# Optimization experiments

Hardware: AMD Instinct MI355X
Metric: run time of the kernel (lower is better)

The kernel has to match this reference:

```python
import jax, jax.numpy as jnp
import numpy as np

B, S, I, H = 64, 2048, 256, 256


def setup_inputs() -> dict:
    key = jax.random.key(0)
    ks = jax.random.split(key, 13)
    s_i = 1.0 / np.sqrt(I)
    s_h = 1.0 / np.sqrt(H)
    inp = {
        "input_seq": jax.random.normal(ks[0], (B, S, I), dtype=jnp.float32),
        "Wz": jax.random.uniform(ks[1], (I, H), jnp.float32, -s_i, s_i),
        "bz": jax.random.uniform(ks[2], (H,), jnp.float32, -s_i, s_i),
        "Wr": jax.random.uniform(ks[3], (I, H), jnp.float32, -s_i, s_i),
        "br": jax.random.uniform(ks[4], (H,), jnp.float32, -s_i, s_i),
        "Wh": jax.random.uniform(ks[5], (I, H), jnp.float32, -s_i, s_i),
        "bh": jax.random.uniform(ks[6], (H,), jnp.float32, -s_i, s_i),
        "Uz": jax.random.uniform(ks[7], (H, H), jnp.float32, -s_h, s_h),
        "buz": jax.random.uniform(ks[8], (H,), jnp.float32, -s_h, s_h),
        "Ur": jax.random.uniform(ks[9], (H, H), jnp.float32, -s_h, s_h),
        "bur": jax.random.uniform(ks[10], (H,), jnp.float32, -s_h, s_h),
        "Uh": jax.random.uniform(ks[11], (H, H), jnp.float32, -s_h, s_h),
        "buh": jax.random.uniform(ks[12], (H,), jnp.float32, -s_h, s_h),
    }
    return inp


def reference(input_seq, Wz, bz, Wr, br, Wh, bh, Uz, buz, Ur, bur, Uh, buh):
    # Precompute all input-side GEMMs in one batched pass: [B,S,H] each
    xz = jnp.einsum("bsi,ih->bsh", input_seq, Wz) + bz
    xr = jnp.einsum("bsi,ih->bsh", input_seq, Wr) + br
    xh = jnp.einsum("bsi,ih->bsh", input_seq, Wh) + bh
    # Time-major for scan: [S,B,H]
    xs = (xz.transpose(1, 0, 2), xr.transpose(1, 0, 2), xh.transpose(1, 0, 2))

    def step(h_prev, x_t):
        xz_t, xr_t, xh_t = x_t
        z = jax.nn.sigmoid(xz_t + h_prev @ Uz + buz)
        r = jax.nn.sigmoid(xr_t + h_prev @ Ur + bur)
        cand = jnp.tanh(xh_t + r * (h_prev @ Uh + buh))
        h_t = (1.0 - z) * h_prev + z * cand
        return h_t, h_t

    h0 = jnp.zeros((input_seq.shape[0], Uz.shape[0]), dtype=input_seq.dtype)
    _, hs = jax.lax.scan(step, h0, xs)  # hs: [S,B,H]
    return hs.transpose(1, 0, 2)  # [B,S,H]
```

## Files before the change

kernel.cpp:

```cpp
#include <hip/hip_runtime.h>
#include <hip/hip_bf16.h>
#include <hip/hip_fp16.h>


#define S_LEN 2048
#define BATCH 64
#define HDIM  256
#define NGATE 768
#define M_TOTAL (BATCH * S_LEN)

typedef _Float16 h8_t __attribute__((ext_vector_type(8)));
typedef float    f32x4 __attribute__((ext_vector_type(4)));
typedef int      i32x4 __attribute__((ext_vector_type(4)));

static __device__ __forceinline__ float h2f(unsigned short s) {
    _Float16 h; __builtin_memcpy(&h, &s, 2); return (float)h;
}
static __device__ __forceinline__ unsigned short f2h(float f) {
    _Float16 h = (_Float16)f; unsigned short s; __builtin_memcpy(&s, &h, 2); return s;
}

static __device__ __forceinline__ float sigmoid_fast(float x) {
    float e = __builtin_amdgcn_exp2f(-1.44269504088896341f * x);
    return __builtin_amdgcn_rcpf(1.0f + e);
}
static __device__ __forceinline__ float tanh_fast(float x) {
    return 2.0f * sigmoid_fast(2.0f * x) - 1.0f;
}


__global__ void k_cvt_x(const float4* __restrict__ x4, ushort4* __restrict__ xh4) {
    int i = blockIdx.x * blockDim.x + threadIdx.x;
    float4 v = x4[i];
    ushort4 o;
    o.x = f2h(v.x); o.y = f2h(v.y); o.z = f2h(v.z); o.w = f2h(v.w);
    xh4[i] = o;
}

__global__ void k_prep_w(const float* __restrict__ Wz, const float* __restrict__ Wr,
                         const float* __restrict__ Wh,
                         const float* __restrict__ bz, const float* __restrict__ br,
                         const float* __restrict__ bh,
                         const float* __restrict__ buz, const float* __restrict__ bur,
                         unsigned short* __restrict__ Wt, float* __restrict__ biascat) {
    int n = blockIdx.x;
    int k = threadIdx.x;
    int g = n >> 8, h = n & 255;
    const float* W = (g == 0) ? Wz : (g == 1) ? Wr : Wh;
    Wt[n * 256 + k] = f2h(W[k * 256 + h]);
    if (k == 0) {
        float bias = (g == 0) ? (bz[h] + buz[h]) : (g == 1) ? (br[h] + bur[h]) : bh[h];
        biascat[n] = bias;
    }
}

__global__ void k_prep_uq(const float* __restrict__ Uz, const float* __restrict__ Ur,
                          const float* __restrict__ Uh,
                          signed char* __restrict__ Ufrag, float* __restrict__ invU) {
    int blk = blockIdx.x;
    int g = blk >> 8, col = blk & 255;
    int k = threadIdx.x;
    const float* U = (g == 0) ? Uz : (g == 1) ? Ur : Uh;
    float v = U[k * 256 + col];
    __shared__ float red[256];
    red[k] = fabsf(v);
    __syncthreads();
    for (int off = 128; off > 0; off >>= 1) {
        if (k < off) red[k] = fmaxf(red[k], red[k + off]);
        __syncthreads();
    }
    float m = red[0];
    float s = (m > 0.0f) ? 127.0f / m : 0.0f;
    int q = __float2int_rn(v * s);
    q = max(-127, min(127, q));
    int ks = k >> 6, l4 = (k >> 4) & 3, e = k & 15;
    int l = l4 * 16 + (col & 15), nt = col >> 4;
    Ufrag[((size_t)(((g * 16 + nt) * 4 + ks) * 64 + l)) * 16 + e] = (signed char)q;
    if (k == 0) invU[g * 256 + col] = m * (1.0f / 16129.0f);
}


#define LDT 264

__global__ __launch_bounds__(256) void k_gemm_x(const unsigned short* __restrict__ Xh,
                                                const unsigned short* __restrict__ Wt,
                                                const float* __restrict__ biascat,
                                                unsigned short* __restrict__ XG) {
    __shared__ unsigned short As[128 * LDT];
    __shared__ unsigned short Bs[128 * LDT];
    int tid = threadIdx.x;
    int m0 = blockIdx.x * 128;
    int n0 = blockIdx.y * 128;

    {
        const unsigned short* ga = Xh + (size_t)m0 * 256;
        const unsigned short* gb = Wt + (size_t)n0 * 256;
#pragma unroll
        for (int i = 0; i < 16; i++) {
            int chunk = tid + i * 256;
            int row = chunk >> 5;
            int c8  = (chunk & 31) * 8;
            uint4 va = *(const uint4*)(ga + row * 256 + c8);
            *(uint4*)(As + row * LDT + c8) = va;
            uint4 vb = *(const uint4*)(gb + row * 256 + c8);
            *(uint4*)(Bs + row * LDT + c8) = vb;
        }
    }
    __syncthreads();

    int lane = tid & 63, wv = tid >> 6;
    int mw = (wv & 1) * 64, nw = (wv >> 1) * 64;
    int lr = lane & 15, lg = lane >> 4;

    f32x4 acc[4][4] = {};
#pragma unroll
    for (int k = 0; k < 8; k++) {
        h8_t a[4], b[4];
#pragma unroll
        for (int i = 0; i < 4; i++)
            a[i] = *(const h8_t*)(As + (mw + i * 16 + lr) * LDT + k * 32 + lg * 8);
#pragma unroll
        for (int jj = 0; jj < 4; jj++)
            b[jj] = *(const h8_t*)(Bs + (nw + jj * 16 + lr) * LDT + k * 32 + lg * 8);
#pragma unroll
        for (int i = 0; i < 4; i++)
#pragma unroll
            for (int jj = 0; jj < 4; jj++)
                acc[i][jj] = __builtin_amdgcn_mfma_f32_16x16x32_f16(a[i], b[jj], acc[i][jj], 0, 0, 0);
    }

#pragma unroll
    for (int jj = 0; jj < 4; jj++) {
        int gcol = n0 + nw + jj * 16 + lr;
        float bias = biascat[gcol];
#pragma unroll
        for (int i = 0; i < 4; i++) {
            int grow = m0 + mw + i * 16 + lg * 4;
#pragma unroll
            for (int r = 0; r < 4; r++) {
                XG[(size_t)(grow + r) * NGATE + gcol] = f2h(acc[i][jj][r] + bias);
            }
        }
    }
}


__global__ __launch_bounds__(1024) __attribute__((amdgpu_waves_per_eu(4, 4)))
void k_gru(const i32x4* __restrict__ Ufrag,
           const float* __restrict__ invU,
           const unsigned short* __restrict__ XG,
           const float* __restrict__ buh,
           float* __restrict__ out) {
    __shared__ __align__(16) signed char hb[2][256];
    int tid = threadIdx.x;
    int lane = tid & 63, w = tid >> 6;
    int l4 = lane >> 4, lc = lane & 15;
    int b = blockIdx.x;
    int c = w * 16 + lc;

    i32x4 uf[3][4];
#pragma unroll
    for (int g = 0; g < 3; g++)
#pragma unroll
        for (int ks = 0; ks < 4; ks++)
            uf[g][ks] = Ufrag[(size_t)((g * 16 + w) * 4 + ks) * 64 + lane];
#pragma unroll
    for (int g = 0; g < 3; g++)
#pragma unroll
        for (int ks = 0; ks < 4; ks++)
            asm volatile("" : "+v"(uf[g][ks]));

    float invz = invU[0 * 256 + c], invr = invU[1 * 256 + c], invh = invU[2 * 256 + c];
    float buh_c = buh[c];

    if (tid < 128) ((int*)hb)[tid] = 0;

    const unsigned short* xb = XG + (size_t)b * S_LEN * NGATE;
    float* ob = out + (size_t)b * S_LEN * HDIM;

    unsigned short pz = xb[0 * 256 + c], pr = xb[1 * 256 + c], ph = xb[2 * 256 + c];
    float hm = 0.0f;
    __syncthreads();

    for (int t = 0; t < S_LEN; ++t) {
        int cur = t & 1;
        const signed char* hrow = hb[cur];

        i32x4 az = {}, ar = {}, ah = {};
        __builtin_amdgcn_s_setprio(1);
#pragma unroll
        for (int ks = 0; ks < 4; ks++) {
            i32x4 a = *(const i32x4*)(hrow + ks * 64 + l4 * 16);
            az = __builtin_amdgcn_mfma_i32_16x16x64_i8(a, uf[0][ks], az, 0, 0, 0);
            ar = __builtin_amdgcn_mfma_i32_16x16x64_i8(a, uf[1][ks], ar, 0, 0, 0);
            ah = __builtin_amdgcn_mfma_i32_16x16x64_i8(a, uf[2][ks], ah, 0, 0, 0);
        }
        __builtin_amdgcn_s_setprio(0);

        float z = sigmoid_fast(h2f(pz) + (float)az[0] * invz);
        float r = sigmoid_fast(h2f(pr) + (float)ar[0] * invr);
        float cd = tanh_fast(h2f(ph) + r * ((float)ah[0] * invh + buh_c));
        hm = (1.0f - z) * hm + z * cd;

        const unsigned short* xn = xb + (size_t)((t + 1 < S_LEN) ? t + 1 : t) * NGATE;
        pz = xn[0 * 256 + c]; pr = xn[1 * 256 + c]; ph = xn[2 * 256 + c];

        if (lane < 16) {
            ob[(size_t)t * HDIM + c] = hm;
            hb[cur ^ 1][c] = (signed char)__float2int_rn(hm * 127.0f);
        }
        __syncthreads();
    }
}


extern "C" void kernel_launch(void* const* d_in, const int* in_sizes, int n_in,
                              void* d_out, int out_size, void* d_ws, size_t ws_size,
                              hipStream_t stream) {
    const float* x   = (const float*)d_in[0];
    const float* Wz  = (const float*)d_in[1];
    const float* bz  = (const float*)d_in[2];
    const float* Wr  = (const float*)d_in[3];
    const float* br  = (const float*)d_in[4];
    const float* Wh  = (const float*)d_in[5];
    const float* bh  = (const float*)d_in[6];
    const float* Uz  = (const float*)d_in[7];
    const float* buz = (const float*)d_in[8];
    const float* Ur  = (const float*)d_in[9];
    const float* bur = (const float*)d_in[10];
    const float* Uh  = (const float*)d_in[11];
    const float* buh = (const float*)d_in[12];

    char* ws = (char*)d_ws;
    unsigned short* Xh = (unsigned short*)(ws);
    unsigned short* XG = (unsigned short*)(ws + 67108864);
    unsigned short* Wt = (unsigned short*)(ws + 268435456);
    signed char*    Ufrag = (signed char*)(ws + 268828672);
    float*          biascat = (float*)(ws + 269221888);
    float*          invU = (float*)(ws + 269225984);

    k_cvt_x<<<32768, 256, 0, stream>>>((const float4*)x, (ushort4*)Xh);
    k_prep_w<<<768, 256, 0, stream>>>(Wz, Wr, Wh, bz, br, bh, buz, bur, Wt, biascat);
    k_prep_uq<<<768, 256, 0, stream>>>(Uz, Ur, Uh, Ufrag, invU);

    dim3 g1(M_TOTAL / 128, NGATE / 128);
    k_gemm_x<<<g1, 256, 0, stream>>>(Xh, Wt, biascat, XG);

    k_gru<<<BATCH, 1024, 0, stream>>>((const i32x4*)Ufrag, invU, XG, buh, (float*)d_out);
}
```

Before: 1.382 ms.

## Skew GRU timestep across two wave groups to overlap gate tail with MFMA

Result: slower. 1.540 ms (+11.4%).

```diff
diff --git a/kernel.cpp b/kernel.cpp
--- a/kernel.cpp
+++ b/kernel.cpp
@@ -157,6 +157,7 @@
     int l4 = lane >> 4, lc = lane & 15;
     int b = blockIdx.x;
     int c = w * 16 + lc;
+    bool grpA = (w < 8);
 
     i32x4 uf[3][4];
 #pragma unroll
@@ -173,44 +174,77 @@
     float invz = invU[0 * 256 + c], invr = invU[1 * 256 + c], invh = invU[2 * 256 + c];
     float buh_c = buh[c];
 
-    if (tid < 128) ((int*)hb)[tid] = 0;
+    if (tid < 64) ((int*)hb[0])[tid] = 0;
 
     const unsigned short* xb = XG + (size_t)b * S_LEN * NGATE;
     float* ob = out + (size_t)b * S_LEN * HDIM;
 
-    unsigned short pz = xb[0 * 256 + c], pr = xb[1 * 256 + c], ph = xb[2 * 256 + c];
+    const unsigned short* xp = xb + c;
+    unsigned short pz = xp[0], pr = xp[256], ph = xp[512];
+    xp += NGATE;
     float hm = 0.0f;
-    __syncthreads();
-
-    for (int t = 0; t < S_LEN; ++t) {
-        int cur = t & 1;
-        const signed char* hrow = hb[cur];
-
-        i32x4 az = {}, ar = {}, ah = {};
+
+    auto mfma2 = [&](i32x4* acc, const signed char* hrow, int ksBase) {
         __builtin_amdgcn_s_setprio(1);
 #pragma unroll
-        for (int ks = 0; ks < 4; ks++) {
+        for (int i = 0; i < 2; i++) {
+            int ks = ksBase + i;
             i32x4 a = *(const i32x4*)(hrow + ks * 64 + l4 * 16);
-            az = __builtin_amdgcn_mfma_i32_16x16x64_i8(a, uf[0][ks], az, 0, 0, 0);
-            ar = __builtin_amdgcn_mfma_i32_16x16x64_i8(a, uf[1][ks], ar, 0, 0, 0);
-            ah = __builtin_amdgcn_mfma_i32_16x16x64_i8(a, uf[2][ks], ah, 0, 0, 0);
+            acc[0] = __builtin_amdgcn_mfma_i32_16x16x64_i8(a, uf[0][ks], acc[0], 0, 0, 0);
+            acc[1] = __builtin_amdgcn_mfma_i32_16x16x64_i8(a, uf[1][ks], acc[1], 0, 0, 0);
+            acc[2] = __builtin_amdgcn_mfma_i32_16x16x64_i8(a, uf[2][ks], acc[2], 0, 0, 0);
         }
         __builtin_amdgcn_s_setprio(0);
-
-        float z = sigmoid_fast(h2f(pz) + (float)az[0] * invz);
-        float r = sigmoid_fast(h2f(pr) + (float)ar[0] * invr);
-        float cd = tanh_fast(h2f(ph) + r * ((float)ah[0] * invh + buh_c));
+    };
+
+    auto tail = [&](const i32x4* acc, int t, signed char* hdst) {
+        float z = sigmoid_fast(h2f(pz) + (float)acc[0][0] * invz);
+        float r = sigmoid_fast(h2f(pr) + (float)acc[1][0] * invr);
+        float cd = tanh_fast(h2f(ph) + r * ((float)acc[2][0] * invh + buh_c));
         hm = (1.0f - z) * hm + z * cd;
-
-        const unsigned short* xn = xb + (size_t)((t + 1 < S_LEN) ? t + 1 : t) * NGATE;
-        pz = xn[0 * 256 + c]; pr = xn[1 * 256 + c]; ph = xn[2 * 256 + c];
-
         if (lane < 16) {
             ob[(size_t)t * HDIM + c] = hm;
-            hb[cur ^ 1][c] = (signed char)__float2int_rn(hm * 127.0f);
-        }
-        __syncthreads();
-    }
+            hdst[c] = (signed char)__float2int_rn(hm * 127.0f);
+        }
+        pz = xp[0]; pr = xp[256]; ph = xp[512];
+        xp += NGATE;
+    };
+
+    i32x4 P[3] = {}, Q[3] = {};
+    __syncthreads();
+
+    mfma2(P, hb[0], 0);
+    mfma2(P, hb[0], 2);
+    if (grpA) tail(P, 0, hb[1]);
+    __syncthreads();
+
+    for (int k = 0; k < 1023; ++k) {
+        int t1 = 2 * k + 1;
+        Q[0] = (i32x4){}; Q[1] = (i32x4){}; Q[2] = (i32x4){};
+        mfma2(Q, hb[1], 0);
+        if (!grpA) tail(P, t1 - 1, hb[1]);
+        __syncthreads();
+        mfma2(Q, hb[1], 2);
+        if (grpA) tail(Q, t1, hb[0]);
+        __syncthreads();
+        P[0] = (i32x4){}; P[1] = (i32x4){}; P[2] = (i32x4){};
+        mfma2(P, hb[0], 0);
+        if (!grpA) tail(Q, t1, hb[0]);
+        __syncthreads();
+        mfma2(P, hb[0], 2);
+        if (grpA) tail(P, t1 + 1, hb[1]);
+        __syncthreads();
+    }
+
+    Q[0] = (i32x4){}; Q[1] = (i32x4){}; Q[2] = (i32x4){};
+    mfma2(Q, hb[1], 0);
+    if (!grpA) tail(P, 2046, hb[1]);
+    __syncthreads();
+    mfma2(Q, hb[1], 2);
+    if (grpA) tail(Q, 2047, hb[0]);
+    __syncthreads();
+
+    if (!grpA) tail(Q, 2047, hb[0]);
 }
 
 
```

## Shrink GRU recurrence block to 4 waves with 4 column tiles each

Applied to the files above, without the earlier changes.

Result: faster. 1.293 ms (-6.4%).

```diff
diff --git a/kernel.cpp b/kernel.cpp
--- a/kernel.cpp
+++ b/kernel.cpp
@@ -145,7 +145,7 @@
 }
 
 
-__global__ __launch_bounds__(1024) __attribute__((amdgpu_waves_per_eu(4, 4)))
+__global__ __launch_bounds__(256) __attribute__((amdgpu_waves_per_eu(1, 1)))
 void k_gru(const i32x4* __restrict__ Ufrag,
            const float* __restrict__ invU,
            const unsigned short* __restrict__ XG,
@@ -156,59 +156,74 @@
     int lane = tid & 63, w = tid >> 6;
     int l4 = lane >> 4, lc = lane & 15;
     int b = blockIdx.x;
-    int c = w * 16 + lc;
-
-    i32x4 uf[3][4];
+    int c = (w * 4 + l4) * 16 + lc;
+
+    i32x4 uf[3][4][4];
 #pragma unroll
     for (int g = 0; g < 3; g++)
 #pragma unroll
-        for (int ks = 0; ks < 4; ks++)
-            uf[g][ks] = Ufrag[(size_t)((g * 16 + w) * 4 + ks) * 64 + lane];
+        for (int i = 0; i < 4; i++)
+#pragma unroll
+            for (int ks = 0; ks < 4; ks++)
+                uf[g][i][ks] = Ufrag[(size_t)((g * 16 + (w * 4 + i)) * 4 + ks) * 64 + lane];
 #pragma unroll
     for (int g = 0; g < 3; g++)
 #pragma unroll
-        for (int ks = 0; ks < 4; ks++)
-            asm volatile("" : "+v"(uf[g][ks]));
+        for (int i = 0; i < 4; i++)
+#pragma unroll
+            for (int ks = 0; ks < 4; ks++)
+                asm volatile("" : "+v"(uf[g][i][ks]));
 
     float invz = invU[0 * 256 + c], invr = invU[1 * 256 + c], invh = invU[2 * 256 + c];
     float buh_c = buh[c];
 
-    if (tid < 128) ((int*)hb)[tid] = 0;
+    if (tid < 64) ((int*)hb[0])[tid] = 0;
 
     const unsigned short* xb = XG + (size_t)b * S_LEN * NGATE;
     float* ob = out + (size_t)b * S_LEN * HDIM;
 
-    unsigned short pz = xb[0 * 256 + c], pr = xb[1 * 256 + c], ph = xb[2 * 256 + c];
+    const unsigned short* xp = xb + c;
+    unsigned short pz = xp[0], pr = xp[256], ph = xp[512];
+    xp += NGATE;
     float hm = 0.0f;
+    bool s0 = (l4 & 1) != 0, s1 = (l4 & 2) != 0;
     __syncthreads();
 
     for (int t = 0; t < S_LEN; ++t) {
-        int cur = t & 1;
-        const signed char* hrow = hb[cur];
-
-        i32x4 az = {}, ar = {}, ah = {};
-        __builtin_amdgcn_s_setprio(1);
+        const signed char* hrow = hb[t & 1];
+        signed char* hdst = hb[(t & 1) ^ 1];
+
+        i32x4 acc[3][4] = {};
 #pragma unroll
         for (int ks = 0; ks < 4; ks++) {
             i32x4 a = *(const i32x4*)(hrow + ks * 64 + l4 * 16);
-            az = __builtin_amdgcn_mfma_i32_16x16x64_i8(a, uf[0][ks], az, 0, 0, 0);
-            ar = __builtin_amdgcn_mfma_i32_16x16x64_i8(a, uf[1][ks], ar, 0, 0, 0);
-            ah = __builtin_amdgcn_mfma_i32_16x16x64_i8(a, uf[2][ks], ah, 0, 0, 0);
+#pragma unroll
+            for (int g = 0; g < 3; g++)
+#pragma unroll
+                for (int i = 0; i < 4; i++)
+                    acc[g][i] = __builtin_amdgcn_mfma_i32_16x16x64_i8(a, uf[g][i][ks], acc[g][i], 0, 0, 0);
         }
-        __builtin_amdgcn_s_setprio(0);
-
-        float z = sigmoid_fast(h2f(pz) + (float)az[0] * invz);
-        float r = sigmoid_fast(h2f(pr) + (float)ar[0] * invr);
-        float cd = tanh_fast(h2f(ph) + r * ((float)ah[0] * invh + buh_c));
+
+        int z01 = s0 ? acc[0][1][0] : acc[0][0][0];
+        int z23 = s0 ? acc[0][3][0] : acc[0][2][0];
+        float vz = (float)(s1 ? z23 : z01) * invz;
+        int r01 = s0 ? acc[1][1][0] : acc[1][0][0];
+        int r23 = s0 ? acc[1][3][0] : acc[1][2][0];
+        float vr = (float)(s1 ? r23 : r01) * invr;
+        int h01 = s0 ? acc[2][1][0] : acc[2][0][0];
+        int h23 = s0 ? acc[2][3][0] : acc[2][2][0];
+        float vh = (float)(s1 ? h23 : h01) * invh;
+
+        float z = sigmoid_fast(h2f(pz) + vz);
+        float r = sigmoid_fast(h2f(pr) + vr);
+        float cd = tanh_fast(h2f(ph) + r * (vh + buh_c));
         hm = (1.0f - z) * hm + z * cd;
 
-        const unsigned short* xn = xb + (size_t)((t + 1 < S_LEN) ? t + 1 : t) * NGATE;
-        pz = xn[0 * 256 + c]; pr = xn[1 * 256 + c]; ph = xn[2 * 256 + c];
-
-        if (lane < 16) {
-            ob[(size_t)t * HDIM + c] = hm;
-            hb[cur ^ 1][c] = (signed char)__float2int_rn(hm * 127.0f);
-        }
+        ob[(size_t)t * HDIM + c] = hm;
+        hdst[c] = (signed char)__float2int_rn(hm * 127.0f);
+
+        pz = xp[0]; pr = xp[256]; ph = xp[512];
+        xp += NGATE;
         __syncthreads();
     }
 }
@@ -246,5 +261,5 @@
     dim3 g1(M_TOTAL / 128, NGATE / 128);
     k_gemm_x<<<g1, 256, 0, stream>>>(Xh, Wt, biascat, XG);
 
-    k_gru<<<BATCH, 1024, 0, stream>>>((const i32x4*)Ufrag, invU, XG, buh, (float*)d_out);
-}
+    k_gru<<<BATCH, 256, 0, stream>>>((const i32x4*)Ufrag, invU, XG, buh, (float*)d_out);
+}
```
